# Kernel optimization log

Measured on AMD Instinct MI355X. Metric: run time of the kernel, lower is better.

The kernel has to match this reference:

```python
import jax, jax.numpy as jnp
import numpy as np

N = 10000      # nodes
E = 65536      # edges
IN = 16        # in_channels
H = 64         # hidden_channels
ED = 4         # edge_attr_dim
MLP_H = 64     # hidden width of edge-weight MLPs


def _glorot(key, shape):
    fan_in, fan_out = shape[0], shape[1]
    lim = np.sqrt(6.0 / (fan_in + fan_out)).astype(np.float32)
    return jax.random.uniform(key, shape, jnp.float32, -lim, lim)


def setup_inputs() -> dict:
    key = jax.random.key(0)
    ks = jax.random.split(key, 16)
    x = jax.random.normal(ks[0], (N, IN), dtype=jnp.float32)
    edge_index = jax.random.randint(ks[1], (2, E), 0, N, dtype=jnp.int64)
    edge_attr = jax.random.normal(ks[2], (E, ED), dtype=jnp.float32)
    return {
        "x": x,
        "edge_index": edge_index,
        "edge_attr": edge_attr,
        # nn1: Linear(ED,64) -> ReLU -> Linear(64, IN*H)
        "nn1_w1": _glorot(ks[3], (ED, MLP_H)), "nn1_b1": jnp.zeros((MLP_H,), jnp.float32),
        "nn1_w2": _glorot(ks[4], (MLP_H, IN * H)), "nn1_b2": jnp.zeros((IN * H,), jnp.float32),
        "root1": _glorot(ks[5], (IN, H)), "bias1": jnp.zeros((H,), jnp.float32),
        # nn2: Linear(ED,64) -> ReLU -> Linear(64, H*H)
        "nn2_w1": _glorot(ks[6], (ED, MLP_H)), "nn2_b1": jnp.zeros((MLP_H,), jnp.float32),
        "nn2_w2": _glorot(ks[7], (MLP_H, H * H)), "nn2_b2": jnp.zeros((H * H,), jnp.float32),
        "root2": _glorot(ks[8], (H, H)), "bias2": jnp.zeros((H,), jnp.float32),
        # readout MLP
        "lin1_w": _glorot(ks[9], (H, 8)), "lin1_b": jnp.zeros((8,), jnp.float32),
        "lin2_w": _glorot(ks[10], (8, 1)), "lin2_b": jnp.zeros((1,), jnp.float32),
    }


def _nnconv(x, src, dst, edge_attr, w1, b1, w2, b2, root, bias, cin, cout):
    # Edge-conditioned weight generation: MLP(edge_attr) -> [E, cin, cout]
    h = jax.nn.relu(edge_attr @ w1 + b1)
    We = (h @ w2 + b2).reshape(-1, cin, cout)
    # Per-edge matmul: message_e = x[src_e] @ We_e  -> [E, cout]
    msg = jnp.einsum('ei,eio->eo', x[src], We)
    # Scatter mean over destination nodes
    s = jax.ops.segment_sum(msg, dst, num_segments=N)
    cnt = jax.ops.segment_sum(jnp.ones((msg.shape[0],), x.dtype), dst, num_segments=N)
    agg = s / jnp.maximum(cnt, 1.0)[:, None]
    # Root transform + bias (PyG NNConv defaults: root_weight=True, bias=True)
    return agg + x @ root + bias


def reference(x, edge_index, edge_attr,
              nn1_w1, nn1_b1, nn1_w2, nn1_b2, root1, bias1,
              nn2_w1, nn2_b1, nn2_w2, nn2_b2, root2, bias2,
              lin1_w, lin1_b, lin2_w, lin2_b):
    # Dropout layers are identity in eval mode.
    src, dst = edge_index[0], edge_index[1]
    h = jax.nn.relu(_nnconv(x, src, dst, edge_attr,
                            nn1_w1, nn1_b1, nn1_w2, nn1_b2, root1, bias1, IN, H))
    h = jax.nn.relu(_nnconv(h, src, dst, edge_attr,
                            nn2_w1, nn2_b1, nn2_w2, nn2_b2, root2, bias2, H, H))
    h = jax.nn.relu(h @ lin1_w + lin1_b)
    return (h @ lin2_w + lin2_b)[:, 0]  # squeeze(-1) -> [N]
```

## Files before the change

### kernel.cpp

```cpp
#include <hip/hip_runtime.h>
#include <hip/hip_bf16.h>

#define NN 10000
#define EE 65536

using short8  = __attribute__((ext_vector_type(8))) short;
using u16x8   = __attribute__((ext_vector_type(8))) unsigned short;
using float4v = __attribute__((ext_vector_type(4))) float;

__device__ __forceinline__ unsigned short f2b(float f){
  union { float f; unsigned int u; } v; v.f = f;
  unsigned int u = v.u;
  unsigned int r = (u + 0x7fff + ((u >> 16) & 1)) >> 16;
  return (unsigned short)r;
}


__device__ __forceinline__ void do_permB(int idx, const float* __restrict__ w2,
                                         unsigned short* __restrict__ Bt, int cin){
  int K = cin*64;
  int o = idx / K;
  int k = idx - o*K;
  int m = k / cin;
  int i = k - m*cin;
  Bt[idx] = f2b(w2[(size_t)m*(cin*64) + i*64 + o]);
}

__global__ __launch_bounds__(256) void k_prep(
    const float* __restrict__ w2a, unsigned short* __restrict__ Bt1,
    const float* __restrict__ w2b, unsigned short* __restrict__ Bt2,
    int* __restrict__ cnt){
  int b = blockIdx.x;
  int t = threadIdx.x;
  if(b < 40){
    int i = b*256 + t;
    if(i < NN) cnt[i] = 0;
  } else if(b < 296){
    do_permB((b-40)*256 + t, w2a, Bt1, 16);
  } else {
    do_permB((b-296)*256 + t, w2b, Bt2, 64);
  }
}


__global__ void k_hist(const int* __restrict__ dst, int* __restrict__ cnt){
  int e = blockIdx.x*256 + threadIdx.x;
  if(e < EE) atomicAdd(&cnt[dst[e]], 1);
}

__global__ __launch_bounds__(1024) void k_scan(const int* __restrict__ cnt, int* __restrict__ offs, int* __restrict__ cursor){
  const int T = 1024, PER = (NN + T - 1)/T;
  int tid = threadIdx.x;
  int base = tid*PER;
  int local[PER];
  int s = 0;
  #pragma unroll
  for(int j=0;j<PER;j++){
    int i = base+j;
    int v = (i<NN)? cnt[i] : 0;
    local[j] = s;
    s += v;
  }
  int lane = tid & 63, wv = tid >> 6;
  int val = s;
  #pragma unroll
  for(int o=1;o<64;o<<=1){
    int u = __shfl_up(val, o, 64);
    if(lane >= o) val += u;
  }
  __shared__ int wsum[16];
  if(lane==63) wsum[wv] = val;
  __syncthreads();
  if(tid==0){
    int acc=0;
    #pragma unroll
    for(int i=0;i<16;i++){ int t2=wsum[i]; wsum[i]=acc; acc+=t2; }
  }
  __syncthreads();
  int thr_excl = wsum[wv] + (val - s);
  #pragma unroll
  for(int j=0;j<PER;j++){
    int i = base+j;
    if(i<NN){ int e = thr_excl + local[j]; offs[i]=e; cursor[i]=e; }
  }
  if(tid == T-1) offs[NN] = thr_excl + s;
}

__global__ void k_scatter(const int* __restrict__ dst, const int* __restrict__ src,
                          int* __restrict__ cursor, int2* __restrict__ elist2){
  int e = blockIdx.x*256 + threadIdx.x;
  if(e < EE){ int p = atomicAdd(&cursor[dst[e]], 1); elist2[p] = make_int2(e, src[e]); }
}


__global__ __launch_bounds__(64) void k_accK1(const float* __restrict__ x,
    const int* __restrict__ offs, const int2* __restrict__ elist2,
    const float* __restrict__ ea, const float* __restrict__ w1, const float* __restrict__ b1,
    unsigned short* __restrict__ K1, float* __restrict__ XS, int v0){
  int v = v0 + blockIdx.x;
  int L = threadIdx.x;
  int cg = L & 3, mg = L >> 2;
  int i0 = cg << 2;
  float w1c0 = w1[L], w1c1 = w1[64+L], w1c2 = w1[128+L], w1c3 = w1[192+L];
  float b1c = b1[L];
  __shared__ float sh[2][64];
  float acc[4][4];
  #pragma unroll
  for(int j=0;j<4;j++)
    #pragma unroll
    for(int c=0;c<4;c++) acc[j][c]=0.f;
  float4 xs = make_float4(0.f,0.f,0.f,0.f);
  int p0 = offs[v], p1 = offs[v+1];
  float4 a_nxt = make_float4(0.f,0.f,0.f,0.f);
  float4 x_nxt = make_float4(0.f,0.f,0.f,0.f);
  if(p0 < p1){
    int2 es = elist2[p0];
    a_nxt = *(const float4*)(ea + (size_t)es.x*4);
    x_nxt = *(const float4*)(x + (size_t)es.y*16 + i0);
  }
  for(int p=p0;p<p1;p++){
    int buf = (p-p0)&1;
    float4 xv = x_nxt;
    float4 av = a_nxt;
    float hv = fmaxf(b1c + av.x*w1c0 + av.y*w1c1 + av.z*w1c2 + av.w*w1c3, 0.f);
    sh[buf][L] = hv;
    __syncthreads();
    if(p+1<p1){
      int2 es = elist2[p+1];
      a_nxt = *(const float4*)(ea + (size_t)es.x*4);
      x_nxt = *(const float4*)(x + (size_t)es.y*16 + i0);
    }
    xs.x += xv.x; xs.y += xv.y; xs.z += xv.z; xs.w += xv.w;
    #pragma unroll
    for(int j=0;j<4;j++){
      float hm = sh[buf][mg + 16*j];
      acc[j][0] += hm*xv.x; acc[j][1] += hm*xv.y;
      acc[j][2] += hm*xv.z; acc[j][3] += hm*xv.w;
    }
  }
  unsigned short* Kv = K1 + (size_t)blockIdx.x*1024;
  #pragma unroll
  for(int j=0;j<4;j++){
    int m = mg + 16*j;
    ushort4 u;
    u.x=f2b(acc[j][0]); u.y=f2b(acc[j][1]); u.z=f2b(acc[j][2]); u.w=f2b(acc[j][3]);
    *(ushort4*)(Kv + m*16 + i0) = u;
  }
  if(mg==0) *(float4*)(XS + (size_t)v*64 + i0) = xs;
}


__global__ __launch_bounds__(64) void k_accK2(const float* __restrict__ x1,
    const int* __restrict__ offs, const int2* __restrict__ elist2,
    const float* __restrict__ ea, const float* __restrict__ w1, const float* __restrict__ b1,
    unsigned short* __restrict__ K, float* __restrict__ XS, int v0){
  int v = v0 + blockIdx.x;
  int L = threadIdx.x;
  int cg = L & 7, mg = L >> 3;
  int i0 = cg << 3;
  float w1c0 = w1[L], w1c1 = w1[64+L], w1c2 = w1[128+L], w1c3 = w1[192+L];
  float b1c = b1[L];
  __shared__ float sh[2][64];
  float acc[8][8];
  #pragma unroll
  for(int j=0;j<8;j++)
    #pragma unroll
    for(int c=0;c<8;c++) acc[j][c]=0.f;
  float4 xs0 = make_float4(0.f,0.f,0.f,0.f);
  float4 xs1 = make_float4(0.f,0.f,0.f,0.f);
  int p0 = offs[v], p1 = offs[v+1];
  float4 a_nxt = make_float4(0.f,0.f,0.f,0.f);
  float4 x_nxt0 = make_float4(0.f,0.f,0.f,0.f);
  float4 x_nxt1 = make_float4(0.f,0.f,0.f,0.f);
  if(p0 < p1){
    int2 es = elist2[p0];
    a_nxt = *(const float4*)(ea + (size_t)es.x*4);
    const float* xr = x1 + (size_t)es.y*64 + i0;
    x_nxt0 = *(const float4*)xr;
    x_nxt1 = *(const float4*)(xr+4);
  }
  for(int p=p0;p<p1;p++){
    int buf = (p-p0)&1;
    float4 xv0 = x_nxt0, xv1 = x_nxt1;
    float4 av = a_nxt;
    float hv = fmaxf(b1c + av.x*w1c0 + av.y*w1c1 + av.z*w1c2 + av.w*w1c3, 0.f);
    sh[buf][L] = hv;
    __syncthreads();
    if(p+1<p1){
      int2 es = elist2[p+1];
      a_nxt = *(const float4*)(ea + (size_t)es.x*4);
      const float* xr = x1 + (size_t)es.y*64 + i0;
      x_nxt0 = *(const float4*)xr;
      x_nxt1 = *(const float4*)(xr+4);
    }
    xs0.x += xv0.x; xs0.y += xv0.y; xs0.z += xv0.z; xs0.w += xv0.w;
    xs1.x += xv1.x; xs1.y += xv1.y; xs1.z += xv1.z; xs1.w += xv1.w;
    float4 h4a = *(float4*)&sh[buf][mg*8];
    float4 h4b = *(float4*)&sh[buf][mg*8+4];
    #pragma unroll
    for(int jj=0;jj<2;jj++){
      float4 h4 = jj? h4b : h4a;
      #pragma unroll
      for(int tq=0;tq<4;tq++){
        int j = jj*4+tq;
        float hm = (tq==0)?h4.x:(tq==1)?h4.y:(tq==2)?h4.z:h4.w;
        acc[j][0] += hm*xv0.x; acc[j][1] += hm*xv0.y;
        acc[j][2] += hm*xv0.z; acc[j][3] += hm*xv0.w;
        acc[j][4] += hm*xv1.x; acc[j][5] += hm*xv1.y;
        acc[j][6] += hm*xv1.z; acc[j][7] += hm*xv1.w;
      }
    }
  }
  unsigned short* Kv = K + (size_t)blockIdx.x*4096;
  #pragma unroll
  for(int j=0;j<8;j++){
    int m = mg*8 + j;
    u16x8 u;
    #pragma unroll
    for(int c=0;c<8;c++) u[c] = f2b(acc[j][c]);
    *(u16x8*)(Kv + m*64 + i0) = u;
  }
  if(mg==0){
    *(float4*)(XS + (size_t)v*64 + i0)     = xs0;
    *(float4*)(XS + (size_t)v*64 + i0 + 4) = xs1;
  }
}


template<int T>
__global__ __launch_bounds__(256) void k_gemm_nl(const unsigned short* __restrict__ A,
    const unsigned short* __restrict__ Bt, float* __restrict__ P,
    int rows, int Ktot){
  int tid = threadIdx.x;
  int lane = tid & 63;
  int w = tid >> 6;
  int rg = blockIdx.x;
  int k0 = blockIdx.y*(4*T*32) + w*(T*32);
  int lrow = lane & 15;
  int lk   = (lane >> 4) << 3;
  const unsigned short* Ap  = A  + (size_t)(rg*16 + lrow)*Ktot + k0 + lk;
  const unsigned short* Bp  = Bt + (size_t)lrow*Ktot + k0 + lk;
  size_t bstep = (size_t)16*Ktot;

  float4v acc0{}, acc1{}, acc2{}, acc3{};
  short8 a_c, b0_c, b1_c, b2_c, b3_c;
  short8 a_n, b0_n, b1_n, b2_n, b3_n;

  a_c  = *(const short8*)(Ap);
  b0_c = *(const short8*)(Bp);
  b1_c = *(const short8*)(Bp + bstep);
  b2_c = *(const short8*)(Bp + bstep*2);
  b3_c = *(const short8*)(Bp + bstep*3);

  #pragma unroll
  for(int t=0; t<T; t++){
    if(t+1 < T){
      a_n  = *(const short8*)(Ap + (t+1)*32);
      b0_n = *(const short8*)(Bp + (t+1)*32);
      b1_n = *(const short8*)(Bp + bstep   + (t+1)*32);
      b2_n = *(const short8*)(Bp + bstep*2 + (t+1)*32);
      b3_n = *(const short8*)(Bp + bstep*3 + (t+1)*32);
    }
    acc0 = __builtin_amdgcn_mfma_f32_16x16x32_bf16(a_c, b0_c, acc0, 0,0,0);
    acc1 = __builtin_amdgcn_mfma_f32_16x16x32_bf16(a_c, b1_c, acc1, 0,0,0);
    acc2 = __builtin_amdgcn_mfma_f32_16x16x32_bf16(a_c, b2_c, acc2, 0,0,0);
    acc3 = __builtin_amdgcn_mfma_f32_16x16x32_bf16(a_c, b3_c, acc3, 0,0,0);
    a_c = a_n; b0_c = b0_n; b1_c = b1_n; b2_c = b2_n; b3_c = b3_n;
  }

  __shared__ float4v sh4[4][4][64];
  sh4[w][0][lane] = acc0;
  sh4[w][1][lane] = acc1;
  sh4[w][2][lane] = acc2;
  sh4[w][3][lane] = acc3;
  __syncthreads();
  float4v r{};
  #pragma unroll
  for(int w2=0; w2<4; w2++){
    float4v v = sh4[w2][w][lane];
    r[0]+=v[0]; r[1]+=v[1]; r[2]+=v[2]; r[3]+=v[3];
  }
  int quad = lane >> 4;
  float* Pr = P + (size_t)blockIdx.y*rows*64 + (size_t)(rg*16 + quad*4)*64 + w*16 + lrow;
  #pragma unroll
  for(int reg=0; reg<4; reg++) Pr[(size_t)reg*64] = r[reg];
}


template<int CIN, int SPLIT>
__global__ __launch_bounds__(256) void k_reduce_ep(const float* __restrict__ P, int rows, int v0,
    const float* __restrict__ XS, const float* __restrict__ b2, const float* __restrict__ xprev,
    const float* __restrict__ root, const float* __restrict__ bias, const int* __restrict__ offs,
    float* __restrict__ out){
  int idx = blockIdx.x*256 + threadIdx.x;
  if(idx >= rows*16) return;
  int r = idx >> 4, og = (idx & 15) << 2;
  int v = v0 + r;

  float4 s = make_float4(0.f,0.f,0.f,0.f);
  #pragma unroll
  for(int z=0; z<SPLIT; z++){
    float4 p = *(const float4*)(P + ((size_t)z*rows + r)*64 + og);
    s.x += p.x; s.y += p.y; s.z += p.z; s.w += p.w;
  }
  #pragma unroll
  for(int i=0;i<CIN;i++){
    float xsv = XS[(size_t)v*64 + i];
    float4 b = *(const float4*)(b2 + i*64 + og);
    s.x += xsv*b.x; s.y += xsv*b.y; s.z += xsv*b.z; s.w += xsv*b.w;
  }
  float4 rt = make_float4(0.f,0.f,0.f,0.f);
  #pragma unroll
  for(int i=0;i<CIN;i++){
    float xv = xprev[(size_t)v*CIN + i];
    float4 wv = *(const float4*)(root + i*64 + og);
    rt.x += xv*wv.x; rt.y += xv*wv.y; rt.z += xv*wv.z; rt.w += xv*wv.w;
  }
  float c = (float)(offs[v+1]-offs[v]); c = fmaxf(c, 1.f);
  float inv = 1.f/c;
  float4 bi = *(const float4*)(bias + og);
  float4 o;
  o.x = fmaxf(s.x*inv + rt.x + bi.x, 0.f);
  o.y = fmaxf(s.y*inv + rt.y + bi.y, 0.f);
  o.z = fmaxf(s.z*inv + rt.z + bi.z, 0.f);
  o.w = fmaxf(s.w*inv + rt.w + bi.w, 0.f);
  *(float4*)(out + (size_t)v*64 + og) = o;
}


template<int SPLIT>
__global__ __launch_bounds__(256) void k_red2_ro(const float* __restrict__ P, int rows,
    const float* __restrict__ XS, const float* __restrict__ b2, const float* __restrict__ x1,
    const float* __restrict__ root, const float* __restrict__ bias, const int* __restrict__ offs,
    const float* __restrict__ lw1, const float* __restrict__ lb1,
    const float* __restrict__ lw2, const float* __restrict__ lb2,
    float* __restrict__ out){
  __shared__ float row[16][68];
  __shared__ float hjs[16][8];
  int tid = threadIdx.x;
  int idx = blockIdx.x*256 + tid;
  int r = idx >> 4, og = (idx & 15) << 2;
  int n = tid >> 4;
  int nbase = blockIdx.x*16;
  int ninblk = rows - nbase; if(ninblk > 16) ninblk = 16;

  float4 o = make_float4(0.f,0.f,0.f,0.f);
  if(r < rows){
    float4 s = make_float4(0.f,0.f,0.f,0.f);
    #pragma unroll
    for(int z=0; z<SPLIT; z++){
      float4 p = *(const float4*)(P + ((size_t)z*rows + r)*64 + og);
      s.x += p.x; s.y += p.y; s.z += p.z; s.w += p.w;
    }
    #pragma unroll
    for(int i=0;i<64;i++){
      float xsv = XS[(size_t)r*64 + i];
      float4 b = *(const float4*)(b2 + i*64 + og);
      s.x += xsv*b.x; s.y += xsv*b.y; s.z += xsv*b.z; s.w += xsv*b.w;
    }
    float4 rt = make_float4(0.f,0.f,0.f,0.f);
    #pragma unroll
    for(int i=0;i<64;i++){
      float xv = x1[(size_t)r*64 + i];
      float4 wv = *(const float4*)(root + i*64 + og);
      rt.x += xv*wv.x; rt.y += xv*wv.y; rt.z += xv*wv.z; rt.w += xv*wv.w;
    }
    float c = (float)(offs[r+1]-offs[r]); c = fmaxf(c, 1.f);
    float inv = 1.f/c;
    float4 bi = *(const float4*)(bias + og);
    o.x = fmaxf(s.x*inv + rt.x + bi.x, 0.f);
    o.y = fmaxf(s.y*inv + rt.y + bi.y, 0.f);
    o.z = fmaxf(s.z*inv + rt.z + bi.z, 0.f);
    o.w = fmaxf(s.w*inv + rt.w + bi.w, 0.f);
  }
  *(float4*)&row[n][og] = o;
  __syncthreads();
  if(tid < 128){
    int n2 = tid >> 3, j = tid & 7;
    if(n2 < ninblk){
      float a = lb1[j];
      #pragma unroll
      for(int i=0;i<64;i++) a += row[n2][i]*lw1[i*8+j];
      hjs[n2][j] = fmaxf(a, 0.f)*lw2[j];
    }
  }
  __syncthreads();
  if(tid < 16 && tid < ninblk){
    float s = lb2[0];
    #pragma unroll
    for(int j=0;j<8;j++) s += hjs[tid][j];
    out[nbase + tid] = s;
  }
}


__global__ void k_readout(const float* __restrict__ x2, const float* __restrict__ lw1,
                          const float* __restrict__ lb1, const float* __restrict__ lw2,
                          const float* __restrict__ lb2, float* __restrict__ out){
  int v = blockIdx.x*256 + threadIdx.x;
  if(v >= NN) return;
  float accj[8];
  #pragma unroll
  for(int j=0;j<8;j++) accj[j] = lb1[j];
  const float* xr = x2 + (size_t)v*64;
  #pragma unroll 16
  for(int i=0;i<64;i++){
    float xv = xr[i];
    #pragma unroll
    for(int j=0;j<8;j++) accj[j] += xv*lw1[i*8+j];
  }
  float o = lb2[0];
  #pragma unroll
  for(int j=0;j<8;j++) o += fmaxf(accj[j],0.f)*lw2[j];
  out[v] = o;
}


extern "C" void kernel_launch(void* const* d_in, const int* in_sizes, int n_in,
                              void* d_out, int out_size, void* d_ws, size_t ws_size,
                              hipStream_t stream) {
  const float* x      = (const float*)d_in[0];
  const int*   ei     = (const int*)d_in[1];
  const float* ea     = (const float*)d_in[2];
  const float* nn1_w1 = (const float*)d_in[3];
  const float* nn1_b1 = (const float*)d_in[4];
  const float* nn1_w2 = (const float*)d_in[5];
  const float* nn1_b2 = (const float*)d_in[6];
  const float* root1  = (const float*)d_in[7];
  const float* bias1  = (const float*)d_in[8];
  const float* nn2_w1 = (const float*)d_in[9];
  const float* nn2_b1 = (const float*)d_in[10];
  const float* nn2_w2 = (const float*)d_in[11];
  const float* nn2_b2 = (const float*)d_in[12];
  const float* root2  = (const float*)d_in[13];
  const float* bias2  = (const float*)d_in[14];
  const float* lin1_w = (const float*)d_in[15];
  const float* lin1_b = (const float*)d_in[16];
  const float* lin2_w = (const float*)d_in[17];
  const float* lin2_b = (const float*)d_in[18];
  float* out = (float*)d_out;

  const int* srcIdx = ei;
  const int* dstIdx = ei + EE;

  char* w = (char*)d_ws;
  size_t off = 0;
  auto alloc = [&](size_t bytes)->void*{
    void* p = w + off;
    off = (off + bytes + 255) & ~(size_t)255;
    return p;
  };
  int*            cnt    = (int*)           alloc((size_t)NN*4);
  int*            offs   = (int*)           alloc((size_t)(NN+1)*4);
  int*            cursor = (int*)           alloc((size_t)NN*4);
  int2*           elist2 = (int2*)          alloc((size_t)EE*8);
  float*          XS     = (float*)         alloc((size_t)NN*64*4);
  float*          x1     = (float*)         alloc((size_t)NN*64*4);
  unsigned short* Bt1    = (unsigned short*)alloc((size_t)64*1024*2);
  unsigned short* Bt2    = (unsigned short*)alloc((size_t)64*4096*2);
  size_t fixedBytes = off;
  size_t R = (ws_size > fixedBytes) ? (ws_size - fixedBytes) : 0;

  const int S1 = 4, S2 = 4;
  size_t needSingle = (size_t)NN*4096*2 + (size_t)S2*NN*64*4;
  bool single = (R >= needSingle + 4096);

  k_prep   <<<1320, 256, 0, stream>>>(nn1_w2, Bt1, nn2_w2, Bt2, cnt);
  k_hist   <<<(EE+255)/256, 256, 0, stream>>>(dstIdx, cnt);
  k_scan   <<<1, 1024, 0, stream>>>(cnt, offs, cursor);
  k_scatter<<<(EE+255)/256, 256, 0, stream>>>(dstIdx, srcIdx, cursor, elist2);

  if(single){
    unsigned short* Kbuf = (unsigned short*)(w + off);
    float* P = (float*)(w + off + (size_t)NN*4096*2);

    k_accK1<<<NN, 64, 0, stream>>>(x, offs, elist2, ea, nn1_w1, nn1_b1, Kbuf, XS, 0);
    {
      dim3 g(NN/16, S1);
      k_gemm_nl<2><<<g, 256, 0, stream>>>(Kbuf, Bt1, P, NN, 1024);
    }
    k_reduce_ep<16,S1><<<(NN*16+255)/256, 256, 0, stream>>>(P, NN, 0, XS, nn1_b2, x,
                                                             root1, bias1, offs, x1);
    k_accK2<<<NN, 64, 0, stream>>>(x1, offs, elist2, ea, nn2_w1, nn2_b1, Kbuf, XS, 0);
    {
      dim3 g(NN/16, S2);
      k_gemm_nl<8><<<g, 256, 0, stream>>>(Kbuf, Bt2, P, NN, 4096);
    }
    k_red2_ro<S2><<<(NN+15)/16, 256, 0, stream>>>(P, NN, XS, nn2_b2, x1, root2, bias2, offs,
                                                   lin1_w, lin1_b, lin2_w, lin2_b, out);
  } else {
    float* x2b = (float*)alloc((size_t)NN*64*4);
    R = (ws_size > off) ? (ws_size - off) : 0;
    long long C2 = (long long)(R / (4096*2 + S2*64*4));
    long long C1 = (long long)(R / (1024*2 + S1*64*4));
    if(C2 > NN) C2 = NN; if(C1 > NN) C1 = NN;
    C2 &= ~63LL; C1 &= ~63LL;
    if(C2 < 128) C2 = 128; if(C1 < 128) C1 = 128;
    unsigned short* Kbuf = (unsigned short*)(w + off);
    {
      float* P = (float*)(w + off + (size_t)C1*1024*2);
      for(long long v0=0; v0<NN; v0+=C1){
        int rows = (int)((NN - v0 < C1) ? (NN - v0) : C1);
        k_accK1<<<rows, 64, 0, stream>>>(x, offs, elist2, ea, nn1_w1, nn1_b1, Kbuf, XS, (int)v0);
        dim3 g(rows/16, S1);
        k_gemm_nl<2><<<g, 256, 0, stream>>>(Kbuf, Bt1, P, rows, 1024);
        k_reduce_ep<16,S1><<<(rows*16+255)/256, 256, 0, stream>>>(P, rows, (int)v0, XS, nn1_b2, x,
                                                                   root1, bias1, offs, x1);
      }
    }
    {
      float* P = (float*)(w + off + (size_t)C2*4096*2);
      for(long long v0=0; v0<NN; v0+=C2){
        int rows = (int)((NN - v0 < C2) ? (NN - v0) : C2);
        k_accK2<<<rows, 64, 0, stream>>>(x1, offs, elist2, ea, nn2_w1, nn2_b1, Kbuf, XS, (int)v0);
        dim3 g(rows/16, S2);
        k_gemm_nl<8><<<g, 256, 0, stream>>>(Kbuf, Bt2, P, rows, 4096);
        k_reduce_ep<64,S2><<<(rows*16+255)/256, 256, 0, stream>>>(P, rows, (int)v0, XS, nn2_b2, x1,
                                                                   root2, bias2, offs, x2b);
      }
    }
    k_readout<<<(NN+255)/256, 256, 0, stream>>>(x2b, lin1_w, lin1_b, lin2_w, lin2_b, out);
  }
}
```

Baseline: 236.9 us.

## Store K and B operands in MFMA fragment-tiled layout for contiguous loads

```diff
diff --git a/kernel.cpp b/kernel.cpp
--- a/kernel.cpp
+++ b/kernel.cpp
@@ -16,13 +16,22 @@
 }
 
 
+
 __device__ __forceinline__ void do_permB(int idx, const float* __restrict__ w2,
-                                         unsigned short* __restrict__ Bt, int cin){
-  int K = cin*64;
-  int o = idx / K;
-  int k = idx - o*K;
-  int m = k / cin;
-  int i = k - m*cin;
+                                         unsigned short* __restrict__ Bt,
+                                         int cin, int s , int cb ){
+  int tile   = idx >> 9;
+  int within = idx & 511;
+  int ot  = tile >> s;
+  int k32 = tile & ((1<<s)-1);
+  int q    = within >> 3;
+  int kklo = within & 7;
+  int orow = q & 15;
+  int kkhi = q >> 4;
+  int o = ot*16 + orow;
+  int k = k32*32 + kkhi*8 + kklo;
+  int m = k >> cb;
+  int i = k & (cin-1);
   Bt[idx] = f2b(w2[(size_t)m*(cin*64) + i*64 + o]);
 }
 
@@ -36,9 +45,9 @@
     int i = b*256 + t;
     if(i < NN) cnt[i] = 0;
   } else if(b < 296){
-    do_permB((b-40)*256 + t, w2a, Bt1, 16);
+    do_permB((b-40)*256 + t, w2a, Bt1, 16, 5, 4);
   } else {
-    do_permB((b-296)*256 + t, w2b, Bt2, 64);
+    do_permB((b-296)*256 + t, w2b, Bt2, 64, 7, 6);
   }
 }
 
@@ -138,13 +147,16 @@
       acc[j][2] += hm*xv.z; acc[j][3] += hm*xv.w;
     }
   }
-  unsigned short* Kv = K1 + (size_t)blockIdx.x*1024;
+  int r = blockIdx.x;
+  int rt = r >> 4, lrow = r & 15;
   #pragma unroll
   for(int j=0;j<4;j++){
     int m = mg + 16*j;
+    size_t sidx = ((size_t)(rt*32 + (m>>1)))*512
+                + (size_t)(((m&1)*2 + (cg>>1))*16 + lrow)*8 + ((cg&1)*4);
     ushort4 u;
     u.x=f2b(acc[j][0]); u.y=f2b(acc[j][1]); u.z=f2b(acc[j][2]); u.w=f2b(acc[j][3]);
-    *(ushort4*)(Kv + m*16 + i0) = u;
+    *(ushort4*)(K1 + sidx) = u;
   }
   if(mg==0) *(float4*)(XS + (size_t)v*64 + i0) = xs;
 }
@@ -211,14 +223,17 @@
       }
     }
   }
-  unsigned short* Kv = K + (size_t)blockIdx.x*4096;
+  int r = blockIdx.x;
+  int rt = r >> 4, lrow = r & 15;
   #pragma unroll
   for(int j=0;j<8;j++){
     int m = mg*8 + j;
+    size_t sidx = ((size_t)(rt*128 + m*2 + (cg>>2)))*512
+                + (size_t)((cg&3)*16 + lrow)*8;
     u16x8 u;
     #pragma unroll
     for(int c=0;c<8;c++) u[c] = f2b(acc[j][c]);
-    *(u16x8*)(Kv + m*64 + i0) = u;
+    *(u16x8*)(K + sidx) = u;
   }
   if(mg==0){
     *(float4*)(XS + (size_t)v*64 + i0)     = xs0;
@@ -230,42 +245,41 @@
 template<int T>
 __global__ __launch_bounds__(256) void k_gemm_nl(const unsigned short* __restrict__ A,
     const unsigned short* __restrict__ Bt, float* __restrict__ P,
-    int rows, int Ktot){
+    int rows, int KT32){
   int tid = threadIdx.x;
   int lane = tid & 63;
   int w = tid >> 6;
   int rg = blockIdx.x;
-  int k0 = blockIdx.y*(4*T*32) + w*(T*32);
-  int lrow = lane & 15;
-  int lk   = (lane >> 4) << 3;
-  const unsigned short* Ap  = A  + (size_t)(rg*16 + lrow)*Ktot + k0 + lk;
-  const unsigned short* Bp  = Bt + (size_t)lrow*Ktot + k0 + lk;
-  size_t bstep = (size_t)16*Ktot;
+  int b32 = (blockIdx.y*4 + w)*T;
+  const unsigned short* Ap = A  + (((size_t)rg*KT32 + b32) << 9) + lane*8;
+  const unsigned short* Bp = Bt + ((size_t)b32 << 9) + lane*8;
+  size_t bstep = (size_t)KT32 << 9;
 
   float4v acc0{}, acc1{}, acc2{}, acc3{};
-  short8 a_c, b0_c, b1_c, b2_c, b3_c;
-  short8 a_n, b0_n, b1_n, b2_n, b3_n;
-
-  a_c  = *(const short8*)(Ap);
-  b0_c = *(const short8*)(Bp);
-  b1_c = *(const short8*)(Bp + bstep);
-  b2_c = *(const short8*)(Bp + bstep*2);
-  b3_c = *(const short8*)(Bp + bstep*3);
-
-  #pragma unroll
-  for(int t=0; t<T; t++){
+
+  short8 a_all[T];
+  #pragma unroll
+  for(int t=0;t<T;t++) a_all[t] = *(const short8*)(Ap + t*512);
+
+  short8 b0_c = *(const short8*)(Bp);
+  short8 b1_c = *(const short8*)(Bp + bstep);
+  short8 b2_c = *(const short8*)(Bp + bstep*2);
+  short8 b3_c = *(const short8*)(Bp + bstep*3);
+
+  #pragma unroll
+  for(int t=0;t<T;t++){
+    short8 b0_n=b0_c, b1_n=b1_c, b2_n=b2_c, b3_n=b3_c;
     if(t+1 < T){
-      a_n  = *(const short8*)(Ap + (t+1)*32);
-      b0_n = *(const short8*)(Bp + (t+1)*32);
-      b1_n = *(const short8*)(Bp + bstep   + (t+1)*32);
-      b2_n = *(const short8*)(Bp + bstep*2 + (t+1)*32);
-      b3_n = *(const short8*)(Bp + bstep*3 + (t+1)*32);
-    }
-    acc0 = __builtin_amdgcn_mfma_f32_16x16x32_bf16(a_c, b0_c, acc0, 0,0,0);
-    acc1 = __builtin_amdgcn_mfma_f32_16x16x32_bf16(a_c, b1_c, acc1, 0,0,0);
-    acc2 = __builtin_amdgcn_mfma_f32_16x16x32_bf16(a_c, b2_c, acc2, 0,0,0);
-    acc3 = __builtin_amdgcn_mfma_f32_16x16x32_bf16(a_c, b3_c, acc3, 0,0,0);
-    a_c = a_n; b0_c = b0_n; b1_c = b1_n; b2_c = b2_n; b3_c = b3_n;
+      b0_n = *(const short8*)(Bp + (t+1)*512);
+      b1_n = *(const short8*)(Bp + bstep   + (t+1)*512);
+      b2_n = *(const short8*)(Bp + bstep*2 + (t+1)*512);
+      b3_n = *(const short8*)(Bp + bstep*3 + (t+1)*512);
+    }
+    acc0 = __builtin_amdgcn_mfma_f32_16x16x32_bf16(a_all[t], b0_c, acc0, 0,0,0);
+    acc1 = __builtin_amdgcn_mfma_f32_16x16x32_bf16(a_all[t], b1_c, acc1, 0,0,0);
+    acc2 = __builtin_amdgcn_mfma_f32_16x16x32_bf16(a_all[t], b2_c, acc2, 0,0,0);
+    acc3 = __builtin_amdgcn_mfma_f32_16x16x32_bf16(a_all[t], b3_c, acc3, 0,0,0);
+    b0_c = b0_n; b1_c = b1_n; b2_c = b2_n; b3_c = b3_n;
   }
 
   __shared__ float4v sh4[4][4][64];
@@ -280,6 +294,7 @@
     float4v v = sh4[w2][w][lane];
     r[0]+=v[0]; r[1]+=v[1]; r[2]+=v[2]; r[3]+=v[3];
   }
+  int lrow = lane & 15;
   int quad = lane >> 4;
   float* Pr = P + (size_t)blockIdx.y*rows*64 + (size_t)(rg*16 + quad*4)*64 + w*16 + lrow;
   #pragma unroll
@@ -477,14 +492,14 @@
     k_accK1<<<NN, 64, 0, stream>>>(x, offs, elist2, ea, nn1_w1, nn1_b1, Kbuf, XS, 0);
     {
       dim3 g(NN/16, S1);
-      k_gemm_nl<2><<<g, 256, 0, stream>>>(Kbuf, Bt1, P, NN, 1024);
+      k_gemm_nl<2><<<g, 256, 0, stream>>>(Kbuf, Bt1, P, NN, 32);
     }
     k_reduce_ep<16,S1><<<(NN*16+255)/256, 256, 0, stream>>>(P, NN, 0, XS, nn1_b2, x,
                                                              root1, bias1, offs, x1);
     k_accK2<<<NN, 64, 0, stream>>>(x1, offs, elist2, ea, nn2_w1, nn2_b1, Kbuf, XS, 0);
     {
       dim3 g(NN/16, S2);
-      k_gemm_nl<8><<<g, 256, 0, stream>>>(Kbuf, Bt2, P, NN, 4096);
+      k_gemm_nl<8><<<g, 256, 0, stream>>>(Kbuf, Bt2, P, NN, 128);
     }
     k_red2_ro<S2><<<(NN+15)/16, 256, 0, stream>>>(P, NN, XS, nn2_b2, x1, root2, bias2, offs,
                                                    lin1_w, lin1_b, lin2_w, lin2_b, out);
@@ -503,7 +518,7 @@
         int rows = (int)((NN - v0 < C1) ? (NN - v0) : C1);
         k_accK1<<<rows, 64, 0, stream>>>(x, offs, elist2, ea, nn1_w1, nn1_b1, Kbuf, XS, (int)v0);
         dim3 g(rows/16, S1);
-        k_gemm_nl<2><<<g, 256, 0, stream>>>(Kbuf, Bt1, P, rows, 1024);
+        k_gemm_nl<2><<<g, 256, 0, stream>>>(Kbuf, Bt1, P, rows, 32);
         k_reduce_ep<16,S1><<<(rows*16+255)/256, 256, 0, stream>>>(P, rows, (int)v0, XS, nn1_b2, x,
                                                                    root1, bias1, offs, x1);
       }
@@ -514,7 +529,7 @@
         int rows = (int)((NN - v0 < C2) ? (NN - v0) : C2);
         k_accK2<<<rows, 64, 0, stream>>>(x1, offs, elist2, ea, nn2_w1, nn2_b1, Kbuf, XS, (int)v0);
         dim3 g(rows/16, S2);
-        k_gemm_nl<8><<<g, 256, 0, stream>>>(Kbuf, Bt2, P, rows, 4096);
+        k_gemm_nl<8><<<g, 256, 0, stream>>>(Kbuf, Bt2, P, rows, 128);
         k_reduce_ep<64,S2><<<(rows*16+255)/256, 256, 0, stream>>>(P, rows, (int)v0, XS, nn2_b2, x1,
                                                                    root2, bias2, offs, x2b);
       }
```

Measured after the change: 253.5 us. 1.07x slower.
